# Kernel tuning notes

Measured on AMD Instinct MI355X. Metric: run time of the kernel, lower is better.

## Reference

```python
import jax, jax.numpy as jnp
import numpy as np

B, T, C = 4, 2048, 1024
H, D = 16, 64  # num_heads, head_dim
SCALE = D ** -0.5


def setup_inputs() -> dict:
    key = jax.random.key(0)
    ks = jax.random.split(key, 6)
    s = 0.02
    return {
        "hidden_states": jax.random.normal(ks[0], (B, T, C), dtype=jnp.float32),
        "wq": jax.random.normal(ks[1], (C, C), dtype=jnp.float32) * s,
        "wk": jax.random.normal(ks[2], (C, C), dtype=jnp.float32) * s,
        "wv": jax.random.normal(ks[3], (C, C), dtype=jnp.float32) * s,
        "wo": jax.random.normal(ks[4], (C, C), dtype=jnp.float32) * s,
        "bo": jnp.zeros((C,), dtype=jnp.float32),
    }


def reference(hidden_states, wq, wk, wv, wo, bo):
    b, t, c = hidden_states.shape
    # torch nn.Linear: y = x @ W^T
    q = hidden_states @ wq.T
    k = hidden_states @ wk.T
    v = hidden_states @ wv.T
    # (b, t, c) -> (b, h, t, d)
    q = q.reshape(b, t, H, D).transpose(0, 2, 1, 3)
    k = k.reshape(b, t, H, D).transpose(0, 2, 1, 3)
    v = v.reshape(b, t, H, D).transpose(0, 2, 1, 3)
    scores = jnp.einsum("bhqd,bhkd->bhqk", q, k) * SCALE
    attn = jax.nn.softmax(scores, axis=-1)
    out = jnp.einsum("bhqk,bhkd->bhqd", attn, v)
    out = out.transpose(0, 2, 1, 3).reshape(b, t, c)
    return out @ wo.T + bo
```

## Files before the change

### kernel.cpp

```cpp
#include <hip/hip_runtime.h>
#include <hip/hip_bf16.h>
#include <stdint.h>
#include <math.h>

#define Bb 4
#define Tt 2048
#define Cc 1024
#define Hh 16
#define Dd 64
#define Mm (Bb * Tt)
#define KVB 64
#define NT (Tt / KVB)

typedef __attribute__((ext_vector_type(8))) short bf8;
typedef __attribute__((ext_vector_type(4))) float f32x4;
typedef __attribute__((ext_vector_type(16))) float f32x16;
typedef __attribute__((ext_vector_type(8))) unsigned short u16x8;

#define QSCALE 0.1803368801111244f

__device__ __forceinline__ unsigned short f2bf(float f) {
  __hip_bfloat16 h = __float2bfloat16(f);
  return *reinterpret_cast<unsigned short*>(&h);
}
__device__ __forceinline__ float bf2f(unsigned short s) {
  union { unsigned u; float f; } v; v.u = ((unsigned)s) << 16;
  return v.f;
}
__device__ __forceinline__ float fexp2(float x) {
#if __has_builtin(__builtin_amdgcn_exp2f)
  return __builtin_amdgcn_exp2f(x);
#else
  return exp2f(x);
#endif
}
__device__ __forceinline__ unsigned cvtpk(float lo, float hi) {
  unsigned r;
  asm volatile("v_cvt_pk_bf16_f32 %0, %1, %2" : "=v"(r) : "v"(lo), "v"(hi));
  return r;
}
__device__ __forceinline__ void gl_lds16(const void* g, void* l) {
  __builtin_amdgcn_global_load_lds(
      (const __attribute__((address_space(1))) void*)g,
      (__attribute__((address_space(3))) void*)l, 16, 0, 0);
}

__global__ __launch_bounds__(256) void cast_all(
    const float* __restrict__ hs, const float* __restrict__ wq,
    const float* __restrict__ wk, const float* __restrict__ wv,
    const float* __restrict__ wo, unsigned short* __restrict__ Xb,
    unsigned short* __restrict__ Wbase) {
  long long g = (long long)(blockIdx.x * 256 + threadIdx.x) * 8;
  const float* src;
  unsigned short* dst;
  long long off;
  const long long HS = 8LL * 1024 * 1024;
  if (g < HS) {
    src = hs; dst = Xb; off = g;
  } else {
    long long r = g - HS;
    int wsel = (int)(r >> 20);
    off = r & ((1LL << 20) - 1);
    src = (wsel == 0) ? wq : (wsel == 1) ? wk : (wsel == 2) ? wv : wo;
    dst = Wbase + ((long long)wsel << 20);
  }
  const float4* p = (const float4*)(src + off);
  float4 a = p[0], b = p[1];
  u16x8 o;
  o[0] = f2bf(a.x); o[1] = f2bf(a.y); o[2] = f2bf(a.z); o[3] = f2bf(a.w);
  o[4] = f2bf(b.x); o[5] = f2bf(b.y); o[6] = f2bf(b.z); o[7] = f2bf(b.w);
  *(u16x8*)(dst + off) = o;
}

template <int MODE>
__global__ __launch_bounds__(256, 2)
void gemm_bt(const unsigned short* __restrict__ A,
             const unsigned short* __restrict__ Bw,
             void* __restrict__ Cout,
             const float* __restrict__ bias,
             int M, int N, int K) {
  __shared__ unsigned short As[128 * 32];
  __shared__ unsigned short Bs[128 * 32];
  const int tid = threadIdx.x;
  const int lane = tid & 63;
  const int w = tid >> 6;
  const int wr = w >> 1, wc = w & 1;
  const int row0 = blockIdx.y * 128;
  const int col0 = blockIdx.x * 128;
  const int lr = lane & 15;
  const int lk = (lane >> 4) * 8;

  f32x4 acc[4][4] = {};

  const int sr = tid >> 2;
  const int sc = (tid & 3) * 8;

  for (int k0 = 0; k0 < K; k0 += 32) {
    gl_lds16(A  + (size_t)(row0 + sr) * K + k0 + sc,      &As[sr * 32 + sc]);
    gl_lds16(A  + (size_t)(row0 + 64 + sr) * K + k0 + sc, &As[(64 + sr) * 32 + sc]);
    gl_lds16(Bw + (size_t)(col0 + sr) * K + k0 + sc,      &Bs[sr * 32 + sc]);
    gl_lds16(Bw + (size_t)(col0 + 64 + sr) * K + k0 + sc, &Bs[(64 + sr) * 32 + sc]);
    __syncthreads();

    bf8 a[4], b[4];
#pragma unroll
    for (int mi = 0; mi < 4; ++mi)
      a[mi] = *(const bf8*)&As[(wr * 64 + mi * 16 + lr) * 32 + lk];
#pragma unroll
    for (int ni = 0; ni < 4; ++ni)
      b[ni] = *(const bf8*)&Bs[(wc * 64 + ni * 16 + lr) * 32 + lk];
#pragma unroll
    for (int mi = 0; mi < 4; ++mi)
#pragma unroll
      for (int ni = 0; ni < 4; ++ni)
        acc[mi][ni] = __builtin_amdgcn_mfma_f32_16x16x32_bf16(
            a[mi], b[ni], acc[mi][ni], 0, 0, 0);
    __syncthreads();
  }

#pragma unroll
  for (int mi = 0; mi < 4; ++mi) {
#pragma unroll
    for (int ni = 0; ni < 4; ++ni) {
      const int col = col0 + wc * 64 + ni * 16 + lr;
      const int rowb = row0 + wr * 64 + mi * 16 + (lane >> 4) * 4;
      if (MODE == 1) {
#pragma unroll
        for (int r = 0; r < 4; ++r)
          ((float*)Cout)[(size_t)(rowb + r) * N + col] = acc[mi][ni][r] + bias[col];
      } else {
        unsigned short* outb = (unsigned short*)Cout;
        if (col < 2048) {
          unsigned short* dst = outb + (col < 1024 ? 0 : 8 * 1024 * 1024);
          const int c = col & 1023;
#pragma unroll
          for (int r = 0; r < 4; ++r)
            dst[(size_t)(rowb + r) * 1024 + c] = f2bf(acc[mi][ni][r]);
        } else {
          const int c = col - 2048;
          const int bidx = rowb >> 11, t0 = rowb & 2047;
          const int hh = c >> 6, dd = c & 63;
          uint2 pk;
          pk.x = (unsigned)f2bf(acc[mi][ni][0]) | ((unsigned)f2bf(acc[mi][ni][1]) << 16);
          pk.y = (unsigned)f2bf(acc[mi][ni][2]) | ((unsigned)f2bf(acc[mi][ni][3]) << 16);
          size_t addr = (((size_t)(bidx * Hh + hh)) * Dd + dd) * (size_t)Tt + t0;
          *(uint2*)(outb + 16 * 1024 * 1024 + addr) = pk;
        }
      }
    }
  }
}

__global__ __launch_bounds__(512, 4)
void flash_attn(const unsigned short* __restrict__ Q,
                const unsigned short* __restrict__ Km,
                const unsigned short* __restrict__ Vt,
                unsigned short* __restrict__ O) {
  __shared__ unsigned short Ks[2][KVB * 64];
  __shared__ unsigned short Vts[2][64 * KVB];

  const int tid = threadIdx.x;
  const int lane = tid & 63;
  const int w = tid >> 6;
  const int bh = blockIdx.x;
  const int qt = blockIdx.y;
  const int b = bh >> 4, h = bh & 15;
  const size_t base = (size_t)b * Tt * Cc + (size_t)h * Dd;
  const size_t vtbase = (size_t)bh * Dd * Tt;
  const int r31 = lane & 31, hi = lane >> 5;
  const int qrow = qt * 256 + w * 32 + r31;
  const int sw = r31 & 7;

  int coh[4];
#pragma unroll
  for (int ks = 0; ks < 4; ++ks) coh[ks] = ((2 * ks + hi) ^ sw) * 8;

  bf8 qb[4];
#pragma unroll
  for (int ks = 0; ks < 4; ++ks) {
    bf8 t = *(const bf8*)(Q + base + (size_t)qrow * Cc + ks * 16 + hi * 8);
#pragma unroll
    for (int i = 0; i < 8; ++i)
      qb[ks][i] = (short)f2bf(bf2f((unsigned short)t[i]) * QSCALE);
  }

  float m_r = -INFINITY, l_r = 0.f;
  f32x16 o_acc[2];
#pragma unroll
  for (int dt = 0; dt < 2; ++dt) o_acc[dt] = (f32x16)0.0f;

  const int strow = tid >> 3;
  const int stch = tid & 7;
  const unsigned short* ksrc = Km + base + (size_t)strow * Cc + ((stch ^ (strow & 7)) * 8);
  const unsigned short* vsrc = Vt + vtbase + (size_t)strow * Tt + ((stch ^ (strow & 7)) * 8);

  gl_lds16(ksrc, &Ks[0][tid * 8]);
  gl_lds16(vsrc, &Vts[0][tid * 8]);
  __syncthreads();

  for (int t = 0; t < NT; ++t) {
    const int cur = t & 1;
    if (t + 1 < NT) {
      const int kb = (t + 1) * KVB;
      gl_lds16(ksrc + (size_t)kb * Cc, &Ks[cur ^ 1][tid * 8]);
      gl_lds16(vsrc + kb,              &Vts[cur ^ 1][tid * 8]);
    }

    f32x16 s[2];
#pragma unroll
    for (int mt = 0; mt < 2; ++mt) {
      f32x16 z = (f32x16)0.0f;
#pragma unroll
      for (int ks = 0; ks < 4; ++ks) {
        bf8 kf = *(const bf8*)&Ks[cur][(mt * 32 + r31) * 64 + coh[ks]];
        z = __builtin_amdgcn_mfma_f32_32x32x16_bf16(kf, qb[ks], z, 0, 0, 0);
      }
      s[mt] = z;
    }

    float a8[8];
#pragma unroll
    for (int mt = 0; mt < 2; ++mt)
#pragma unroll
      for (int g = 0; g < 4; ++g)
        a8[mt * 4 + g] = fmaxf(fmaxf(s[mt][4 * g], s[mt][4 * g + 1]),
                               fmaxf(s[mt][4 * g + 2], s[mt][4 * g + 3]));
    float mx = fmaxf(fmaxf(fmaxf(a8[0], a8[1]), fmaxf(a8[2], a8[3])),
                     fmaxf(fmaxf(a8[4], a8[5]), fmaxf(a8[6], a8[7])));
    mx = fmaxf(mx, __shfl_xor(mx, 32));

    if (__any(mx > m_r + 8.0f)) {
      float mn = fmaxf(m_r, mx);
      float alpha = fexp2(m_r - mn);
      m_r = mn;
      l_r *= alpha;
#pragma unroll
      for (int dt = 0; dt < 2; ++dt)
#pragma unroll
        for (int j = 0; j < 16; ++j) o_acc[dt][j] *= alpha;
    }

#pragma unroll
    for (int mt = 0; mt < 2; ++mt)
#pragma unroll
      for (int j = 0; j < 16; ++j) s[mt][j] = fexp2(s[mt][j] - m_r);

    float q0 = 0.f, q1 = 0.f, q2 = 0.f, q3 = 0.f;
#pragma unroll
    for (int mt = 0; mt < 2; ++mt)
#pragma unroll
      for (int j = 0; j < 16; j += 4) {
        q0 += s[mt][j]; q1 += s[mt][j + 1]; q2 += s[mt][j + 2]; q3 += s[mt][j + 3];
      }
    float ps = (q0 + q1) + (q2 + q3);
    ps += __shfl_xor(ps, 32);
    l_r += ps;

    unsigned U[8][2];
#pragma unroll
    for (int k = 0; k < 8; ++k) {
      U[k][0] = cvtpk(s[k >> 2][4 * (k & 3)],     s[k >> 2][4 * (k & 3) + 1]);
      U[k][1] = cvtpk(s[k >> 2][4 * (k & 3) + 2], s[k >> 2][4 * (k & 3) + 3]);
    }
    bf8 pb[4];
#pragma unroll
    for (int ks = 0; ks < 4; ++ks) {
      unsigned a0 = U[2 * ks][0], b0 = U[2 * ks + 1][0];
      asm volatile("v_permlane32_swap_b32 %0, %1" : "+v"(a0), "+v"(b0));
      unsigned a1 = U[2 * ks][1], b1 = U[2 * ks + 1][1];
      asm volatile("v_permlane32_swap_b32 %0, %1" : "+v"(a1), "+v"(b1));
      union { unsigned u[4]; bf8 v; } pk_;
      pk_.u[0] = a0; pk_.u[1] = a1; pk_.u[2] = b0; pk_.u[3] = b1;
      pb[ks] = pk_.v;
    }

#pragma unroll
    for (int dt = 0; dt < 2; ++dt) {
      f32x16 z = o_acc[dt];
#pragma unroll
      for (int ks = 0; ks < 4; ++ks) {
        bf8 vf = *(const bf8*)&Vts[cur][(dt * 32 + r31) * 64 + coh[ks]];
        z = __builtin_amdgcn_mfma_f32_32x32x16_bf16(vf, pb[ks], z, 0, 0, 0);
      }
      o_acc[dt] = z;
    }
    __syncthreads();
  }

  const float linv = 1.0f / l_r;
#pragma unroll
  for (int dt = 0; dt < 2; ++dt)
#pragma unroll
    for (int g = 0; g < 4; ++g) {
      uint2 pk;
      pk.x = (unsigned)f2bf(o_acc[dt][4 * g] * linv) |
             ((unsigned)f2bf(o_acc[dt][4 * g + 1] * linv) << 16);
      pk.y = (unsigned)f2bf(o_acc[dt][4 * g + 2] * linv) |
             ((unsigned)f2bf(o_acc[dt][4 * g + 3] * linv) << 16);
      *(uint2*)(O + base + (size_t)qrow * Cc + dt * 32 + g * 8 + hi * 4) = pk;
    }
}

extern "C" void kernel_launch(void* const* d_in, const int* in_sizes, int n_in,
                              void* d_out, int out_size, void* d_ws, size_t ws_size,
                              hipStream_t stream) {
  (void)in_sizes; (void)n_in; (void)out_size; (void)ws_size;
  const float* hs = (const float*)d_in[0];
  const float* wq = (const float*)d_in[1];
  const float* wk = (const float*)d_in[2];
  const float* wv = (const float*)d_in[3];
  const float* wo = (const float*)d_in[4];
  const float* bo = (const float*)d_in[5];

  char* ws = (char*)d_ws;
  const size_t MB = 1u << 20;
  unsigned short* Xb  = (unsigned short*)(ws + 0);
  unsigned short* Wqb = (unsigned short*)(ws + 16 * MB);
  unsigned short* Wob = (unsigned short*)(ws + 22 * MB);
  unsigned short* Qb  = (unsigned short*)(ws + 24 * MB);
  unsigned short* Kb  = (unsigned short*)(ws + 40 * MB);
  unsigned short* Vtb = (unsigned short*)(ws + 56 * MB);
  unsigned short* Ob  = Xb;

  cast_all<<<6144, 256, 0, stream>>>(hs, wq, wk, wv, wo, Xb, Wqb);

  gemm_bt<3><<<dim3(24, 64), 256, 0, stream>>>(Xb, Wqb, Qb, nullptr, Mm, 3072, Cc);

  flash_attn<<<dim3(Bb * Hh, Tt / 256), 512, 0, stream>>>(Qb, Kb, Vtb, Ob);

  gemm_bt<1><<<dim3(8, 64), 256, 0, stream>>>(Ob, Wob, (float*)d_out, bo, Mm, Cc, Cc);
}
```

Baseline: 199.5 us.

## Process two query tiles per wave in flash attention with 256-thread blocks

Each wave now handles 64 query rows as two 32-row tiles, sharing every K and V LDS fragment load across two MFMAs. Blocks shrink from 512 to 256 threads, so each thread issues two async global-to-LDS copies per K/V tile. The max reduction uses v_max3 and the row sum uses vector adds. The aim is to cut LDS reads per MFMA and give the scheduler two independent softmax chains to interleave, at the cost of roughly doubled accumulator registers and lower occupancy.

```diff
diff --git a/kernel.cpp b/kernel.cpp
--- a/kernel.cpp
+++ b/kernel.cpp
@@ -15,6 +15,8 @@
 typedef __attribute__((ext_vector_type(8))) short bf8;
 typedef __attribute__((ext_vector_type(4))) float f32x4;
 typedef __attribute__((ext_vector_type(16))) float f32x16;
+typedef __attribute__((ext_vector_type(8))) float f32x8v;
+typedef __attribute__((ext_vector_type(2))) float f32x2v;
 typedef __attribute__((ext_vector_type(8))) unsigned short u16x8;
 
 #define QSCALE 0.1803368801111244f
@@ -33,6 +35,11 @@
 #else
   return exp2f(x);
 #endif
+}
+__device__ __forceinline__ float fmax3(float a, float b, float c) {
+  float r;
+  asm("v_max3_f32 %0, %1, %2, %3" : "=v"(r) : "v"(a), "v"(b), "v"(c));
+  return r;
 }
 __device__ __forceinline__ unsigned cvtpk(float lo, float hi) {
   unsigned r;
@@ -151,7 +158,7 @@
   }
 }
 
-__global__ __launch_bounds__(512, 4)
+__global__ __launch_bounds__(256, 2)
 void flash_attn(const unsigned short* __restrict__ Q,
                 const unsigned short* __restrict__ Km,
                 const unsigned short* __restrict__ Vt,
@@ -168,137 +175,162 @@
   const size_t base = (size_t)b * Tt * Cc + (size_t)h * Dd;
   const size_t vtbase = (size_t)bh * Dd * Tt;
   const int r31 = lane & 31, hi = lane >> 5;
-  const int qrow = qt * 256 + w * 32 + r31;
+  const int qrowA = qt * 256 + w * 64 + r31;
+  const int qrowB = qrowA + 32;
   const int sw = r31 & 7;
 
   int coh[4];
 #pragma unroll
   for (int ks = 0; ks < 4; ++ks) coh[ks] = ((2 * ks + hi) ^ sw) * 8;
 
-  bf8 qb[4];
+  bf8 qbA[4], qbB[4];
 #pragma unroll
   for (int ks = 0; ks < 4; ++ks) {
-    bf8 t = *(const bf8*)(Q + base + (size_t)qrow * Cc + ks * 16 + hi * 8);
-#pragma unroll
-    for (int i = 0; i < 8; ++i)
-      qb[ks][i] = (short)f2bf(bf2f((unsigned short)t[i]) * QSCALE);
-  }
-
-  float m_r = -INFINITY, l_r = 0.f;
-  f32x16 o_acc[2];
-#pragma unroll
-  for (int dt = 0; dt < 2; ++dt) o_acc[dt] = (f32x16)0.0f;
+    bf8 tA = *(const bf8*)(Q + base + (size_t)qrowA * Cc + ks * 16 + hi * 8);
+    bf8 tB = *(const bf8*)(Q + base + (size_t)qrowB * Cc + ks * 16 + hi * 8);
+#pragma unroll
+    for (int i = 0; i < 8; ++i) {
+      qbA[ks][i] = (short)f2bf(bf2f((unsigned short)tA[i]) * QSCALE);
+      qbB[ks][i] = (short)f2bf(bf2f((unsigned short)tB[i]) * QSCALE);
+    }
+  }
+
+  float m_rA = -INFINITY, l_rA = 0.f, m_rB = -INFINITY, l_rB = 0.f;
+  f32x16 oA[2], oB[2];
+#pragma unroll
+  for (int dt = 0; dt < 2; ++dt) { oA[dt] = (f32x16)0.0f; oB[dt] = (f32x16)0.0f; }
 
   const int strow = tid >> 3;
   const int stch = tid & 7;
   const unsigned short* ksrc = Km + base + (size_t)strow * Cc + ((stch ^ (strow & 7)) * 8);
   const unsigned short* vsrc = Vt + vtbase + (size_t)strow * Tt + ((stch ^ (strow & 7)) * 8);
 
-  gl_lds16(ksrc, &Ks[0][tid * 8]);
-  gl_lds16(vsrc, &Vts[0][tid * 8]);
+  gl_lds16(ksrc,                   &Ks[0][tid * 8]);
+  gl_lds16(ksrc + (size_t)32 * Cc, &Ks[0][tid * 8 + 2048]);
+  gl_lds16(vsrc,                   &Vts[0][tid * 8]);
+  gl_lds16(vsrc + (size_t)32 * Tt, &Vts[0][tid * 8 + 2048]);
   __syncthreads();
 
   for (int t = 0; t < NT; ++t) {
     const int cur = t & 1;
     if (t + 1 < NT) {
       const int kb = (t + 1) * KVB;
-      gl_lds16(ksrc + (size_t)kb * Cc, &Ks[cur ^ 1][tid * 8]);
-      gl_lds16(vsrc + kb,              &Vts[cur ^ 1][tid * 8]);
-    }
-
-    f32x16 s[2];
-#pragma unroll
-    for (int mt = 0; mt < 2; ++mt) {
-      f32x16 z = (f32x16)0.0f;
-#pragma unroll
-      for (int ks = 0; ks < 4; ++ks) {
-        bf8 kf = *(const bf8*)&Ks[cur][(mt * 32 + r31) * 64 + coh[ks]];
-        z = __builtin_amdgcn_mfma_f32_32x32x16_bf16(kf, qb[ks], z, 0, 0, 0);
-      }
-      s[mt] = z;
-    }
-
-    float a8[8];
-#pragma unroll
-    for (int mt = 0; mt < 2; ++mt)
-#pragma unroll
-      for (int g = 0; g < 4; ++g)
-        a8[mt * 4 + g] = fmaxf(fmaxf(s[mt][4 * g], s[mt][4 * g + 1]),
-                               fmaxf(s[mt][4 * g + 2], s[mt][4 * g + 3]));
-    float mx = fmaxf(fmaxf(fmaxf(a8[0], a8[1]), fmaxf(a8[2], a8[3])),
-                     fmaxf(fmaxf(a8[4], a8[5]), fmaxf(a8[6], a8[7])));
-    mx = fmaxf(mx, __shfl_xor(mx, 32));
-
-    if (__any(mx > m_r + 8.0f)) {
-      float mn = fmaxf(m_r, mx);
-      float alpha = fexp2(m_r - mn);
-      m_r = mn;
-      l_r *= alpha;
-#pragma unroll
-      for (int dt = 0; dt < 2; ++dt)
-#pragma unroll
-        for (int j = 0; j < 16; ++j) o_acc[dt][j] *= alpha;
-    }
-
-#pragma unroll
-    for (int mt = 0; mt < 2; ++mt)
-#pragma unroll
-      for (int j = 0; j < 16; ++j) s[mt][j] = fexp2(s[mt][j] - m_r);
-
-    float q0 = 0.f, q1 = 0.f, q2 = 0.f, q3 = 0.f;
-#pragma unroll
-    for (int mt = 0; mt < 2; ++mt)
-#pragma unroll
-      for (int j = 0; j < 16; j += 4) {
-        q0 += s[mt][j]; q1 += s[mt][j + 1]; q2 += s[mt][j + 2]; q3 += s[mt][j + 3];
-      }
-    float ps = (q0 + q1) + (q2 + q3);
-    ps += __shfl_xor(ps, 32);
-    l_r += ps;
-
-    unsigned U[8][2];
-#pragma unroll
-    for (int k = 0; k < 8; ++k) {
-      U[k][0] = cvtpk(s[k >> 2][4 * (k & 3)],     s[k >> 2][4 * (k & 3) + 1]);
-      U[k][1] = cvtpk(s[k >> 2][4 * (k & 3) + 2], s[k >> 2][4 * (k & 3) + 3]);
-    }
-    bf8 pb[4];
+      gl_lds16(ksrc + (size_t)kb * Cc,        &Ks[cur ^ 1][tid * 8]);
+      gl_lds16(ksrc + (size_t)(kb + 32) * Cc, &Ks[cur ^ 1][tid * 8 + 2048]);
+      gl_lds16(vsrc + kb,                     &Vts[cur ^ 1][tid * 8]);
+      gl_lds16(vsrc + kb + (size_t)32 * Tt,   &Vts[cur ^ 1][tid * 8 + 2048]);
+    }
+
+    f32x16 sA0 = (f32x16)0.0f, sA1 = (f32x16)0.0f;
+    f32x16 sB0 = (f32x16)0.0f, sB1 = (f32x16)0.0f;
 #pragma unroll
     for (int ks = 0; ks < 4; ++ks) {
-      unsigned a0 = U[2 * ks][0], b0 = U[2 * ks + 1][0];
-      asm volatile("v_permlane32_swap_b32 %0, %1" : "+v"(a0), "+v"(b0));
-      unsigned a1 = U[2 * ks][1], b1 = U[2 * ks + 1][1];
-      asm volatile("v_permlane32_swap_b32 %0, %1" : "+v"(a1), "+v"(b1));
-      union { unsigned u[4]; bf8 v; } pk_;
-      pk_.u[0] = a0; pk_.u[1] = a1; pk_.u[2] = b0; pk_.u[3] = b1;
-      pb[ks] = pk_.v;
-    }
+      bf8 kf = *(const bf8*)&Ks[cur][r31 * 64 + coh[ks]];
+      sA0 = __builtin_amdgcn_mfma_f32_32x32x16_bf16(kf, qbA[ks], sA0, 0, 0, 0);
+      sB0 = __builtin_amdgcn_mfma_f32_32x32x16_bf16(kf, qbB[ks], sB0, 0, 0, 0);
+    }
+#pragma unroll
+    for (int ks = 0; ks < 4; ++ks) {
+      bf8 kf = *(const bf8*)&Ks[cur][(32 + r31) * 64 + coh[ks]];
+      sA1 = __builtin_amdgcn_mfma_f32_32x32x16_bf16(kf, qbA[ks], sA1, 0, 0, 0);
+      sB1 = __builtin_amdgcn_mfma_f32_32x32x16_bf16(kf, qbB[ks], sB1, 0, 0, 0);
+    }
+
+    bf8 pbA[4], pbB[4];
+#define SOFTMAX_PACK(s0, s1, m_r, l_r, oacc, pb)                              \
+    {                                                                          \
+      float t0 = fmax3(s0[0], s0[1], s0[2]);                                   \
+      float t1 = fmax3(s0[3], s0[4], s0[5]);                                   \
+      float t2 = fmax3(s0[6], s0[7], s0[8]);                                   \
+      float t3 = fmax3(s0[9], s0[10], s0[11]);                                 \
+      float t4 = fmax3(s0[12], s0[13], s0[14]);                                \
+      float t5 = fmax3(s0[15], s1[0], s1[1]);                                  \
+      float t6 = fmax3(s1[2], s1[3], s1[4]);                                   \
+      float t7 = fmax3(s1[5], s1[6], s1[7]);                                   \
+      float t8 = fmax3(s1[8], s1[9], s1[10]);                                  \
+      float t9 = fmax3(s1[11], s1[12], s1[13]);                                \
+      float t10 = fmaxf(s1[14], s1[15]);                                       \
+      float u0 = fmax3(t0, t1, t2);                                            \
+      float u1 = fmax3(t3, t4, t5);                                            \
+      float u2 = fmax3(t6, t7, t8);                                            \
+      float mx = fmaxf(fmax3(u0, u1, u2), fmaxf(t9, t10));                     \
+      mx = fmaxf(mx, __shfl_xor(mx, 32));                                      \
+      if (__any(mx > m_r + 8.0f)) {                                            \
+        float mn = fmaxf(m_r, mx);                                             \
+        float alpha = fexp2(m_r - mn);                                         \
+        m_r = mn;                                                              \
+        l_r *= alpha;                                                          \
+        oacc[0] *= alpha;                                                      \
+        oacc[1] *= alpha;                                                      \
+      }                                                                        \
+      s0 = s0 - m_r;                                                           \
+      s1 = s1 - m_r;                                                           \
+      _Pragma("unroll")                                                        \
+      for (int j = 0; j < 16; ++j) { s0[j] = fexp2(s0[j]); s1[j] = fexp2(s1[j]); } \
+      {                                                                        \
+        f32x16 t16 = s0 + s1;                                                  \
+        f32x8v t8v = __builtin_shufflevector(t16, t16, 0, 1, 2, 3, 4, 5, 6, 7) + \
+                     __builtin_shufflevector(t16, t16, 8, 9, 10, 11, 12, 13, 14, 15); \
+        f32x4 t4v = __builtin_shufflevector(t8v, t8v, 0, 1, 2, 3) +            \
+                    __builtin_shufflevector(t8v, t8v, 4, 5, 6, 7);             \
+        f32x2v t2v = __builtin_shufflevector(t4v, t4v, 0, 1) +                 \
+                     __builtin_shufflevector(t4v, t4v, 2, 3);                  \
+        float ps = t2v[0] + t2v[1];                                            \
+        ps += __shfl_xor(ps, 32);                                              \
+        l_r += ps;                                                             \
+      }                                                                        \
+      unsigned U[8][2];                                                        \
+      _Pragma("unroll")                                                        \
+      for (int k = 0; k < 4; ++k) {                                            \
+        U[k][0] = cvtpk(s0[4 * k], s0[4 * k + 1]);                             \
+        U[k][1] = cvtpk(s0[4 * k + 2], s0[4 * k + 3]);                         \
+        U[4 + k][0] = cvtpk(s1[4 * k], s1[4 * k + 1]);                         \
+        U[4 + k][1] = cvtpk(s1[4 * k + 2], s1[4 * k + 3]);                     \
+      }                                                                        \
+      _Pragma("unroll")                                                        \
+      for (int ks = 0; ks < 4; ++ks) {                                         \
+        unsigned a0 = U[2 * ks][0], b0 = U[2 * ks + 1][0];                     \
+        asm volatile("v_permlane32_swap_b32 %0, %1" : "+v"(a0), "+v"(b0));     \
+        unsigned a1 = U[2 * ks][1], b1 = U[2 * ks + 1][1];                     \
+        asm volatile("v_permlane32_swap_b32 %0, %1" : "+v"(a1), "+v"(b1));     \
+        union { unsigned u[4]; bf8 v; } pk_;                                   \
+        pk_.u[0] = a0; pk_.u[1] = a1; pk_.u[2] = b0; pk_.u[3] = b1;            \
+        pb[ks] = pk_.v;                                                        \
+      }                                                                        \
+    }
+    SOFTMAX_PACK(sA0, sA1, m_rA, l_rA, oA, pbA)
+    SOFTMAX_PACK(sB0, sB1, m_rB, l_rB, oB, pbB)
+#undef SOFTMAX_PACK
 
 #pragma unroll
     for (int dt = 0; dt < 2; ++dt) {
-      f32x16 z = o_acc[dt];
+      f32x16 zA = oA[dt], zB = oB[dt];
 #pragma unroll
       for (int ks = 0; ks < 4; ++ks) {
         bf8 vf = *(const bf8*)&Vts[cur][(dt * 32 + r31) * 64 + coh[ks]];
-        z = __builtin_amdgcn_mfma_f32_32x32x16_bf16(vf, pb[ks], z, 0, 0, 0);
+        zA = __builtin_amdgcn_mfma_f32_32x32x16_bf16(vf, pbA[ks], zA, 0, 0, 0);
+        zB = __builtin_amdgcn_mfma_f32_32x32x16_bf16(vf, pbB[ks], zB, 0, 0, 0);
       }
-      o_acc[dt] = z;
+      oA[dt] = zA; oB[dt] = zB;
     }
     __syncthreads();
   }
 
-  const float linv = 1.0f / l_r;
-#pragma unroll
-  for (int dt = 0; dt < 2; ++dt)
+  const float liA = 1.0f / l_rA, liB = 1.0f / l_rB;
+#pragma unroll
+  for (int dt = 0; dt < 2; ++dt) {
+    f32x16 nA = oA[dt] * liA, nB = oB[dt] * liB;
 #pragma unroll
     for (int g = 0; g < 4; ++g) {
-      uint2 pk;
-      pk.x = (unsigned)f2bf(o_acc[dt][4 * g] * linv) |
-             ((unsigned)f2bf(o_acc[dt][4 * g + 1] * linv) << 16);
-      pk.y = (unsigned)f2bf(o_acc[dt][4 * g + 2] * linv) |
-             ((unsigned)f2bf(o_acc[dt][4 * g + 3] * linv) << 16);
-      *(uint2*)(O + base + (size_t)qrow * Cc + dt * 32 + g * 8 + hi * 4) = pk;
-    }
+      uint2 pkA, pkB;
+      pkA.x = (unsigned)f2bf(nA[4 * g]) | ((unsigned)f2bf(nA[4 * g + 1]) << 16);
+      pkA.y = (unsigned)f2bf(nA[4 * g + 2]) | ((unsigned)f2bf(nA[4 * g + 3]) << 16);
+      pkB.x = (unsigned)f2bf(nB[4 * g]) | ((unsigned)f2bf(nB[4 * g + 1]) << 16);
+      pkB.y = (unsigned)f2bf(nB[4 * g + 2]) | ((unsigned)f2bf(nB[4 * g + 3]) << 16);
+      *(uint2*)(O + base + (size_t)qrowA * Cc + dt * 32 + g * 8 + hi * 4) = pkA;
+      *(uint2*)(O + base + (size_t)qrowB * Cc + dt * 32 + g * 8 + hi * 4) = pkB;
+    }
+  }
 }
 
 extern "C" void kernel_launch(void* const* d_in, const int* in_sizes, int n_in,
@@ -326,7 +358,7 @@
 
   gemm_bt<3><<<dim3(24, 64), 256, 0, stream>>>(Xb, Wqb, Qb, nullptr, Mm, 3072, Cc);
 
-  flash_attn<<<dim3(Bb * Hh, Tt / 256), 512, 0, stream>>>(Qb, Kb, Vtb, Ob);
+  flash_attn<<<dim3(Bb * Hh, Tt / 256), 256, 0, stream>>>(Qb, Kb, Vtb, Ob);
 
   gemm_bt<1><<<dim3(8, 64), 256, 0, stream>>>(Ob, Wob, (float*)d_out, bo, Mm, Cc, Cc);
 }
```

Result: no change. 201.4 us (+1.0%).
